# Kernel tuning notes

Measured on AMD Instinct MI355X. Metric: run time of the kernel, lower is better.

The kernel has to match this reference:

```python
import jax, jax.numpy as jnp
import numpy as np

D_HEAD = 64

def setup_inputs() -> dict:
    key = jax.random.key(0)
    ks = jax.random.split(key, 5)
    B, N, d_feat, d = 8, 2048, 256, 3
    f = jax.random.normal(ks[0], (B, N, d_feat), dtype=jnp.float32)
    x_tilde = jax.random.normal(ks[1], (B, N, d), dtype=jnp.float32)
    log_eps = jax.random.normal(ks[2], (B,), dtype=jnp.float32)
    W_q = jax.random.normal(ks[3], (d_feat + 1, D_HEAD), dtype=jnp.float32) * (1.0 / np.sqrt(d_feat + 1))
    W_k = jax.random.normal(ks[4], (d_feat + 1, D_HEAD), dtype=jnp.float32) * (1.0 / np.sqrt(d_feat + 1))
    return {"f": f, "x_tilde": x_tilde, "log_eps": log_eps, "W_q": W_q, "W_k": W_k}

def reference(f, x_tilde, log_eps, W_q, W_k):
    B, N, _ = f.shape
    # concat per-cloud log_eps scalar to every particle's features
    le = jnp.broadcast_to(log_eps[:, None, None], (B, N, 1)).astype(f.dtype)
    fc = jnp.concatenate([f, le], axis=-1)            # (B, N, d_feat+1)
    q = jnp.einsum('bnf,fh->bnh', fc, W_q)            # (B, N, d_head)
    k = jnp.einsum('bnf,fh->bnh', fc, W_k)            # (B, N, d_head)
    scale = jnp.asarray(np.sqrt(float(D_HEAD)), dtype=f.dtype)
    logits = jnp.einsum('bnh,bmh->bnm', q, k) / scale  # (B, N, N)
    N_f = jnp.asarray(N, dtype=f.dtype)
    col_softmax = jax.nn.softmax(logits, axis=1)       # softmax over QUERY axis
    pi = col_softmax / N_f                             # (B, N, N)
    # y_tilde = N * pi^T @ x_tilde
    y_tilde = N_f * jnp.einsum('bnm,bnd->bmd', pi, x_tilde)  # (B, N, d)
    return y_tilde, pi
```

## Files before the change

### kernel.cpp

```cpp
#include <hip/hip_runtime.h>
#include <hip/hip_bf16.h>

#define BB 8
#define NN 2048
#define DF 256
#define HH 64

using bf16x8 = __attribute__((ext_vector_type(8))) short;
using f32x4  = __attribute__((ext_vector_type(4))) float;
typedef unsigned short u16;

__global__ __launch_bounds__(256) void qk_proj_kernel(
    const float* __restrict__ f, const float* __restrict__ log_eps,
    const float* __restrict__ Wq, const float* __restrict__ Wk,
    __hip_bfloat16* __restrict__ Qs, __hip_bfloat16* __restrict__ Ks)
{
    __shared__ float wql[64 * 64];
    __shared__ float wkl[64 * 64];
    const int tid = threadIdx.x;
    const int h  = tid & 63;
    const int rg = tid >> 6;
    const int row_base = blockIdx.x * 32;
    const int b = row_base >> 11;

    const float le = log_eps[b];
    const float wq_last = Wq[DF * HH + h];
    const float wk_last = Wk[DF * HH + h];
    float q[8], k[8];
#pragma unroll
    for (int j = 0; j < 8; ++j) { q[j] = le * wq_last; k[j] = le * wk_last; }

    for (int kc = 0; kc < 4; ++kc) {
        __syncthreads();
#pragma unroll
        for (int it = 0; it < 4; ++it) {
            int idx = (tid + it * 256) * 4;
            *(float4*)&wql[idx] = *(const float4*)(Wq + kc * 4096 + idx);
            *(float4*)&wkl[idx] = *(const float4*)(Wk + kc * 4096 + idx);
        }
        __syncthreads();

        const float* fb = f + (size_t)(row_base + rg * 8) * DF + kc * 64;
#pragma unroll 4
        for (int i4 = 0; i4 < 16; ++i4) {
            float4 fv[8];
#pragma unroll
            for (int j = 0; j < 8; ++j)
                fv[j] = *(const float4*)(fb + (size_t)j * DF + i4 * 4);
#pragma unroll
            for (int u = 0; u < 4; ++u) {
                float wq = wql[(i4 * 4 + u) * 64 + h];
                float wk = wkl[(i4 * 4 + u) * 64 + h];
#pragma unroll
                for (int j = 0; j < 8; ++j) {
                    float fvv = (&fv[j].x)[u];
                    q[j] = fmaf(fvv, wq, q[j]);
                    k[j] = fmaf(fvv, wk, k[j]);
                }
            }
        }
    }

#pragma unroll
    for (int j = 0; j < 8; ++j) {
        int bn = row_base + rg * 8 + j;
        float qv = q[j] * 0.125f;
        float kv = k[j];
        __hip_bfloat16 qh = __float2bfloat16(qv);
        __hip_bfloat16 ql = __float2bfloat16(qv - __bfloat162float(qh));
        __hip_bfloat16 kh = __float2bfloat16(kv);
        __hip_bfloat16 kl = __float2bfloat16(kv - __bfloat162float(kh));
        size_t base = (size_t)bn * 128;
        Qs[base + h]      = qh;
        Qs[base + 64 + h] = ql;
        Ks[base + h]      = kh;
        Ks[base + 64 + h] = kl;
    }
}

__global__ __launch_bounds__(256) void attn_kernel(
    const u16* __restrict__ Qs, const u16* __restrict__ Ks,
    const float* __restrict__ x, float* __restrict__ y, float* __restrict__ pi)
{
    __shared__ float xs[NN * 3];
    __shared__ float cs_lds[32];
    __shared__ float yred[4 * 2 * 16 * 3];

    const int tid   = threadIdx.x;
    const int strip = blockIdx.x;
    const int b     = blockIdx.y;
    const int m0    = strip * 32;
    const int wave  = tid >> 6;
    const int lane  = tid & 63;
    const int l15   = lane & 15;
    const int quad  = lane >> 4;

    if (tid < 32) cs_lds[tid] = 0.f;
    for (int i = tid; i < NN * 3; i += 256) xs[i] = x[(size_t)b * NN * 3 + i];
    __syncthreads();

    bf16x8 bh[2][2], bl[2][2];
    {
        const u16* Kb = Ks + ((size_t)b * NN + m0) * 128;
#pragma unroll
        for (int ct = 0; ct < 2; ++ct) {
            const u16* kr = Kb + (size_t)(ct * 16 + l15) * 128;
#pragma unroll
            for (int ks = 0; ks < 2; ++ks) {
                int k0 = ks * 32 + quad * 8;
                bh[ct][ks] = *(const bf16x8*)(kr + k0);
                bl[ct][ks] = *(const bf16x8*)(kr + 64 + k0);
            }
        }
    }

    const u16* Qb = Qs + (size_t)b * NN * 128;
    float csacc0 = 0.f, csacc1 = 0.f;

    for (int rt = 0; rt < 16; ++rt) {
#pragma unroll
        for (int sr = 0; sr < 2; ++sr) {
            const int row0 = rt * 128 + wave * 32 + sr * 16;
            const u16* qr = Qb + (size_t)(row0 + l15) * 128;
            bf16x8 ah[2], al[2];
#pragma unroll
            for (int ks = 0; ks < 2; ++ks) {
                int k0 = ks * 32 + quad * 8;
                ah[ks] = *(const bf16x8*)(qr + k0);
                al[ks] = *(const bf16x8*)(qr + 64 + k0);
            }
#pragma unroll
            for (int ct = 0; ct < 2; ++ct) {
                f32x4 acc = {0.f, 0.f, 0.f, 0.f};
#pragma unroll
                for (int ks = 0; ks < 2; ++ks) {
                    acc = __builtin_amdgcn_mfma_f32_16x16x32_bf16(ah[ks], bh[ct][ks], acc, 0, 0, 0);
                    acc = __builtin_amdgcn_mfma_f32_16x16x32_bf16(ah[ks], bl[ct][ks], acc, 0, 0, 0);
                    acc = __builtin_amdgcn_mfma_f32_16x16x32_bf16(al[ks], bh[ct][ks], acc, 0, 0, 0);
                }
                float s = __expf(acc[0]) + __expf(acc[1]) + __expf(acc[2]) + __expf(acc[3]);
                s += __shfl_xor(s, 16);
                s += __shfl_xor(s, 32);
                if (ct == 0) csacc0 += s; else csacc1 += s;
            }
        }
    }
    if (quad == 0) {
        atomicAdd(&cs_lds[l15],      csacc0);
        atomicAdd(&cs_lds[16 + l15], csacc1);
    }
    __syncthreads();

    const float invc0 = 1.0f / cs_lds[l15];
    const float invc1 = 1.0f / cs_lds[16 + l15];
    const float invN  = 1.0f / (float)NN;
    float* pib = pi + (size_t)b * NN * NN + m0;
    float yacc[2][3] = {{0.f, 0.f, 0.f}, {0.f, 0.f, 0.f}};

    for (int rt = 0; rt < 16; ++rt) {
#pragma unroll
        for (int sr = 0; sr < 2; ++sr) {
            const int row0 = rt * 128 + wave * 32 + sr * 16;
            const u16* qr = Qb + (size_t)(row0 + l15) * 128;
            bf16x8 ah[2], al[2];
#pragma unroll
            for (int ks = 0; ks < 2; ++ks) {
                int k0 = ks * 32 + quad * 8;
                ah[ks] = *(const bf16x8*)(qr + k0);
                al[ks] = *(const bf16x8*)(qr + 64 + k0);
            }
            float xv[4][3];
#pragma unroll
            for (int r = 0; r < 4; ++r) {
                int row = row0 + quad * 4 + r;
                xv[r][0] = xs[row * 3 + 0];
                xv[r][1] = xs[row * 3 + 1];
                xv[r][2] = xs[row * 3 + 2];
            }
#pragma unroll
            for (int ct = 0; ct < 2; ++ct) {
                f32x4 acc = {0.f, 0.f, 0.f, 0.f};
#pragma unroll
                for (int ks = 0; ks < 2; ++ks) {
                    acc = __builtin_amdgcn_mfma_f32_16x16x32_bf16(ah[ks], bh[ct][ks], acc, 0, 0, 0);
                    acc = __builtin_amdgcn_mfma_f32_16x16x32_bf16(ah[ks], bl[ct][ks], acc, 0, 0, 0);
                    acc = __builtin_amdgcn_mfma_f32_16x16x32_bf16(al[ks], bh[ct][ks], acc, 0, 0, 0);
                }
                const float iv = (ct == 0) ? invc0 : invc1;
                float* op = pib + (size_t)(row0 + quad * 4) * NN + ct * 16 + l15;
#pragma unroll
                for (int r = 0; r < 4; ++r) {
                    float v = __expf(acc[r]) * iv;
                    op[(size_t)r * NN] = v * invN;
                    yacc[ct][0] = fmaf(v, xv[r][0], yacc[ct][0]);
                    yacc[ct][1] = fmaf(v, xv[r][1], yacc[ct][1]);
                    yacc[ct][2] = fmaf(v, xv[r][2], yacc[ct][2]);
                }
            }
        }
    }

#pragma unroll
    for (int ct = 0; ct < 2; ++ct)
#pragma unroll
        for (int d = 0; d < 3; ++d) {
            yacc[ct][d] += __shfl_xor(yacc[ct][d], 16);
            yacc[ct][d] += __shfl_xor(yacc[ct][d], 32);
        }
    if (quad == 0) {
#pragma unroll
        for (int ct = 0; ct < 2; ++ct)
#pragma unroll
            for (int d = 0; d < 3; ++d)
                yred[((wave * 2 + ct) * 16 + l15) * 3 + d] = yacc[ct][d];
    }
    __syncthreads();
    if (tid < 96) {
        int c = tid / 3, d = tid - c * 3;
        int ct = c >> 4, cl = c & 15;
        float s = 0.f;
#pragma unroll
        for (int w = 0; w < 4; ++w)
            s += yred[((w * 2 + ct) * 16 + cl) * 3 + d];
        y[((size_t)b * NN + m0 + c) * 3 + d] = s;
    }
}

extern "C" void kernel_launch(void* const* d_in, const int* in_sizes, int n_in,
                              void* d_out, int out_size, void* d_ws, size_t ws_size,
                              hipStream_t stream) {
    const float* f  = (const float*)d_in[0];
    const float* x  = (const float*)d_in[1];
    const float* le = (const float*)d_in[2];
    const float* Wq = (const float*)d_in[3];
    const float* Wk = (const float*)d_in[4];

    float* y  = (float*)d_out;
    float* pi = (float*)d_out + (size_t)BB * NN * 3;

    __hip_bfloat16* Qs = (__hip_bfloat16*)d_ws;
    __hip_bfloat16* Ks = Qs + (size_t)BB * NN * 128;

    qk_proj_kernel<<<dim3(BB * NN / 32), 256, 0, stream>>>(f, le, Wq, Wk, Qs, Ks);
    attn_kernel<<<dim3(64, BB), 256, 0, stream>>>((const u16*)Qs, (const u16*)Ks, x, y, pi);
}
```

Baseline: 240.2 us.

## Split attention into colsum and pi/y kernels over row tiles with atomics

The single attention kernel, which ran 512 blocks each looping over all query rows twice, becomes two kernels launched over 64x8xB grids. A colsum kernel accumulates column exp-sums into global memory with atomics, and a pi_y kernel recomputes logits per 256-row tile, writes pi as vectorized float4 stores along m, and atomically adds partial y. The MFMA operands are swapped so each lane owns contiguous columns for the wider stores. The projection kernel also halves its rows per block to launch more blocks. This adds two memsets, an extra launch and global atomics in exchange for much more parallelism and coalesced pi writes.

```diff
diff --git a/kernel.cpp b/kernel.cpp
--- a/kernel.cpp
+++ b/kernel.cpp
@@ -20,15 +20,15 @@
     const int tid = threadIdx.x;
     const int h  = tid & 63;
     const int rg = tid >> 6;
-    const int row_base = blockIdx.x * 32;
+    const int row_base = blockIdx.x * 16;
     const int b = row_base >> 11;
 
     const float le = log_eps[b];
     const float wq_last = Wq[DF * HH + h];
     const float wk_last = Wk[DF * HH + h];
-    float q[8], k[8];
-#pragma unroll
-    for (int j = 0; j < 8; ++j) { q[j] = le * wq_last; k[j] = le * wk_last; }
+    float q[4], k[4];
+#pragma unroll
+    for (int j = 0; j < 4; ++j) { q[j] = le * wq_last; k[j] = le * wk_last; }
 
     for (int kc = 0; kc < 4; ++kc) {
         __syncthreads();
@@ -40,19 +40,19 @@
         }
         __syncthreads();
 
-        const float* fb = f + (size_t)(row_base + rg * 8) * DF + kc * 64;
-#pragma unroll 4
+        const float* fb = f + (size_t)(row_base + rg * 4) * DF + kc * 64;
+#pragma unroll 8
         for (int i4 = 0; i4 < 16; ++i4) {
-            float4 fv[8];
-#pragma unroll
-            for (int j = 0; j < 8; ++j)
+            float4 fv[4];
+#pragma unroll
+            for (int j = 0; j < 4; ++j)
                 fv[j] = *(const float4*)(fb + (size_t)j * DF + i4 * 4);
 #pragma unroll
             for (int u = 0; u < 4; ++u) {
                 float wq = wql[(i4 * 4 + u) * 64 + h];
                 float wk = wkl[(i4 * 4 + u) * 64 + h];
 #pragma unroll
-                for (int j = 0; j < 8; ++j) {
+                for (int j = 0; j < 4; ++j) {
                     float fvv = (&fv[j].x)[u];
                     q[j] = fmaf(fvv, wq, q[j]);
                     k[j] = fmaf(fvv, wk, k[j]);
@@ -62,8 +62,8 @@
     }
 
 #pragma unroll
-    for (int j = 0; j < 8; ++j) {
-        int bn = row_base + rg * 8 + j;
+    for (int j = 0; j < 4; ++j) {
+        int bn = row_base + rg * 4 + j;
         float qv = q[j] * 0.125f;
         float kv = k[j];
         __hip_bfloat16 qh = __float2bfloat16(qv);
@@ -78,25 +78,21 @@
     }
 }
 
-__global__ __launch_bounds__(256) void attn_kernel(
+__global__ __launch_bounds__(256) void colsum_kernel(
     const u16* __restrict__ Qs, const u16* __restrict__ Ks,
-    const float* __restrict__ x, float* __restrict__ y, float* __restrict__ pi)
+    float* __restrict__ cs)
 {
-    __shared__ float xs[NN * 3];
     __shared__ float cs_lds[32];
-    __shared__ float yred[4 * 2 * 16 * 3];
-
-    const int tid   = threadIdx.x;
-    const int strip = blockIdx.x;
-    const int b     = blockIdx.y;
-    const int m0    = strip * 32;
-    const int wave  = tid >> 6;
-    const int lane  = tid & 63;
-    const int l15   = lane & 15;
-    const int quad  = lane >> 4;
+    const int tid  = threadIdx.x;
+    const int m0   = blockIdx.x * 32;
+    const int rt   = blockIdx.y;
+    const int b    = blockIdx.z;
+    const int wave = tid >> 6;
+    const int lane = tid & 63;
+    const int l15  = lane & 15;
+    const int quad = lane >> 4;
 
     if (tid < 32) cs_lds[tid] = 0.f;
-    for (int i = tid; i < NN * 3; i += 256) xs[i] = x[(size_t)b * NN * 3 + i];
     __syncthreads();
 
     bf16x8 bh[2][2], bl[2][2];
@@ -115,114 +111,156 @@
     }
 
     const u16* Qb = Qs + (size_t)b * NN * 128;
-    float csacc0 = 0.f, csacc1 = 0.f;
-
-    for (int rt = 0; rt < 16; ++rt) {
-#pragma unroll
-        for (int sr = 0; sr < 2; ++sr) {
-            const int row0 = rt * 128 + wave * 32 + sr * 16;
-            const u16* qr = Qb + (size_t)(row0 + l15) * 128;
-            bf16x8 ah[2], al[2];
+    float cs0 = 0.f, cs1 = 0.f;
+#pragma unroll
+    for (int sr = 0; sr < 4; ++sr) {
+        const int row0 = rt * 256 + wave * 64 + sr * 16;
+        const u16* qr = Qb + (size_t)(row0 + l15) * 128;
+        bf16x8 ah[2], al[2];
+#pragma unroll
+        for (int ks = 0; ks < 2; ++ks) {
+            int k0 = ks * 32 + quad * 8;
+            ah[ks] = *(const bf16x8*)(qr + k0);
+            al[ks] = *(const bf16x8*)(qr + 64 + k0);
+        }
+#pragma unroll
+        for (int ct = 0; ct < 2; ++ct) {
+            f32x4 acc = {0.f, 0.f, 0.f, 0.f};
+#pragma unroll
+            for (int ks = 0; ks < 2; ++ks) {
+                acc = __builtin_amdgcn_mfma_f32_16x16x32_bf16(ah[ks], bh[ct][ks], acc, 0, 0, 0);
+                acc = __builtin_amdgcn_mfma_f32_16x16x32_bf16(ah[ks], bl[ct][ks], acc, 0, 0, 0);
+                acc = __builtin_amdgcn_mfma_f32_16x16x32_bf16(al[ks], bh[ct][ks], acc, 0, 0, 0);
+            }
+            float s = __expf(acc[0]) + __expf(acc[1]) + __expf(acc[2]) + __expf(acc[3]);
+            s += __shfl_xor(s, 16);
+            s += __shfl_xor(s, 32);
+            if (ct == 0) cs0 += s; else cs1 += s;
+        }
+    }
+    if (quad == 0) {
+        atomicAdd(&cs_lds[l15],      cs0);
+        atomicAdd(&cs_lds[16 + l15], cs1);
+    }
+    __syncthreads();
+    if (tid < 32) atomicAdd(&cs[(size_t)b * NN + m0 + tid], cs_lds[tid]);
+}
+
+__global__ __launch_bounds__(256) void pi_y_kernel(
+    const u16* __restrict__ Qs, const u16* __restrict__ Ks,
+    const float* __restrict__ x, const float* __restrict__ cs,
+    float* __restrict__ y, float* __restrict__ pi)
+{
+    __shared__ float xt[256 * 3];
+    __shared__ float iv_lds[32], ivn_lds[32];
+    __shared__ float yred[4][32][3];
+
+    const int tid  = threadIdx.x;
+    const int m0   = blockIdx.x * 32;
+    const int rt   = blockIdx.y;
+    const int b    = blockIdx.z;
+    const int n0   = rt * 256;
+    const int wave = tid >> 6;
+    const int lane = tid & 63;
+    const int l15  = lane & 15;
+    const int quad = lane >> 4;
+
+    for (int i = tid; i < 256 * 3; i += 256) xt[i] = x[((size_t)b * NN + n0) * 3 + i];
+    if (tid < 32) {
+        float iv = 1.0f / cs[(size_t)b * NN + m0 + tid];
+        iv_lds[tid]  = iv;
+        ivn_lds[tid] = iv * (1.0f / (float)NN);
+    }
+    __syncthreads();
+
+    bf16x8 kh[2][2], kl[2][2];
+    {
+        const u16* Kb = Ks + ((size_t)b * NN + m0) * 128;
+#pragma unroll
+        for (int ct = 0; ct < 2; ++ct) {
+            const u16* kr = Kb + (size_t)(ct * 16 + l15) * 128;
 #pragma unroll
             for (int ks = 0; ks < 2; ++ks) {
                 int k0 = ks * 32 + quad * 8;
-                ah[ks] = *(const bf16x8*)(qr + k0);
-                al[ks] = *(const bf16x8*)(qr + 64 + k0);
-            }
-#pragma unroll
-            for (int ct = 0; ct < 2; ++ct) {
-                f32x4 acc = {0.f, 0.f, 0.f, 0.f};
-#pragma unroll
-                for (int ks = 0; ks < 2; ++ks) {
-                    acc = __builtin_amdgcn_mfma_f32_16x16x32_bf16(ah[ks], bh[ct][ks], acc, 0, 0, 0);
-                    acc = __builtin_amdgcn_mfma_f32_16x16x32_bf16(ah[ks], bl[ct][ks], acc, 0, 0, 0);
-                    acc = __builtin_amdgcn_mfma_f32_16x16x32_bf16(al[ks], bh[ct][ks], acc, 0, 0, 0);
-                }
-                float s = __expf(acc[0]) + __expf(acc[1]) + __expf(acc[2]) + __expf(acc[3]);
-                s += __shfl_xor(s, 16);
-                s += __shfl_xor(s, 32);
-                if (ct == 0) csacc0 += s; else csacc1 += s;
-            }
-        }
-    }
-    if (quad == 0) {
-        atomicAdd(&cs_lds[l15],      csacc0);
-        atomicAdd(&cs_lds[16 + l15], csacc1);
-    }
-    __syncthreads();
-
-    const float invc0 = 1.0f / cs_lds[l15];
-    const float invc1 = 1.0f / cs_lds[16 + l15];
-    const float invN  = 1.0f / (float)NN;
-    float* pib = pi + (size_t)b * NN * NN + m0;
-    float yacc[2][3] = {{0.f, 0.f, 0.f}, {0.f, 0.f, 0.f}};
-
-    for (int rt = 0; rt < 16; ++rt) {
-#pragma unroll
-        for (int sr = 0; sr < 2; ++sr) {
-            const int row0 = rt * 128 + wave * 32 + sr * 16;
-            const u16* qr = Qb + (size_t)(row0 + l15) * 128;
-            bf16x8 ah[2], al[2];
-#pragma unroll
-            for (int ks = 0; ks < 2; ++ks) {
-                int k0 = ks * 32 + quad * 8;
-                ah[ks] = *(const bf16x8*)(qr + k0);
-                al[ks] = *(const bf16x8*)(qr + 64 + k0);
-            }
-            float xv[4][3];
+                kh[ct][ks] = *(const bf16x8*)(kr + k0);
+                kl[ct][ks] = *(const bf16x8*)(kr + 64 + k0);
+            }
+        }
+    }
+
+    const u16* Qb = Qs + (size_t)b * NN * 128;
+    float yacc[2][4][3];
+#pragma unroll
+    for (int ct = 0; ct < 2; ++ct)
+#pragma unroll
+        for (int r = 0; r < 4; ++r)
+#pragma unroll
+            for (int d = 0; d < 3; ++d) yacc[ct][r][d] = 0.f;
+
+#pragma unroll
+    for (int sr = 0; sr < 4; ++sr) {
+        const int nloc = wave * 64 + sr * 16 + l15;
+        const u16* qr = Qb + (size_t)(n0 + nloc) * 128;
+        bf16x8 qh[2], ql[2];
+#pragma unroll
+        for (int ks = 0; ks < 2; ++ks) {
+            int k0 = ks * 32 + quad * 8;
+            qh[ks] = *(const bf16x8*)(qr + k0);
+            ql[ks] = *(const bf16x8*)(qr + 64 + k0);
+        }
+        const float xv0 = xt[nloc * 3 + 0];
+        const float xv1 = xt[nloc * 3 + 1];
+        const float xv2 = xt[nloc * 3 + 2];
+#pragma unroll
+        for (int ct = 0; ct < 2; ++ct) {
+            f32x4 acc = {0.f, 0.f, 0.f, 0.f};
+#pragma unroll
+            for (int ks = 0; ks < 2; ++ks) {
+                acc = __builtin_amdgcn_mfma_f32_16x16x32_bf16(kh[ct][ks], qh[ks], acc, 0, 0, 0);
+                acc = __builtin_amdgcn_mfma_f32_16x16x32_bf16(kh[ct][ks], ql[ks], acc, 0, 0, 0);
+                acc = __builtin_amdgcn_mfma_f32_16x16x32_bf16(kl[ct][ks], qh[ks], acc, 0, 0, 0);
+            }
+            const int mloc = ct * 16 + quad * 4;
+            f32x4 pv;
 #pragma unroll
             for (int r = 0; r < 4; ++r) {
-                int row = row0 + quad * 4 + r;
-                xv[r][0] = xs[row * 3 + 0];
-                xv[r][1] = xs[row * 3 + 1];
-                xv[r][2] = xs[row * 3 + 2];
-            }
-#pragma unroll
-            for (int ct = 0; ct < 2; ++ct) {
-                f32x4 acc = {0.f, 0.f, 0.f, 0.f};
-#pragma unroll
-                for (int ks = 0; ks < 2; ++ks) {
-                    acc = __builtin_amdgcn_mfma_f32_16x16x32_bf16(ah[ks], bh[ct][ks], acc, 0, 0, 0);
-                    acc = __builtin_amdgcn_mfma_f32_16x16x32_bf16(ah[ks], bl[ct][ks], acc, 0, 0, 0);
-                    acc = __builtin_amdgcn_mfma_f32_16x16x32_bf16(al[ks], bh[ct][ks], acc, 0, 0, 0);
-                }
-                const float iv = (ct == 0) ? invc0 : invc1;
-                float* op = pib + (size_t)(row0 + quad * 4) * NN + ct * 16 + l15;
-#pragma unroll
-                for (int r = 0; r < 4; ++r) {
-                    float v = __expf(acc[r]) * iv;
-                    op[(size_t)r * NN] = v * invN;
-                    yacc[ct][0] = fmaf(v, xv[r][0], yacc[ct][0]);
-                    yacc[ct][1] = fmaf(v, xv[r][1], yacc[ct][1]);
-                    yacc[ct][2] = fmaf(v, xv[r][2], yacc[ct][2]);
-                }
-            }
+                float e = __expf(acc[r]);
+                pv[r] = e * ivn_lds[mloc + r];
+                yacc[ct][r][0] = fmaf(e, xv0, yacc[ct][r][0]);
+                yacc[ct][r][1] = fmaf(e, xv1, yacc[ct][r][1]);
+                yacc[ct][r][2] = fmaf(e, xv2, yacc[ct][r][2]);
+            }
+            *(f32x4*)(pi + ((size_t)b * NN + n0 + nloc) * NN + m0 + mloc) = pv;
         }
     }
 
 #pragma unroll
     for (int ct = 0; ct < 2; ++ct)
 #pragma unroll
-        for (int d = 0; d < 3; ++d) {
-            yacc[ct][d] += __shfl_xor(yacc[ct][d], 16);
-            yacc[ct][d] += __shfl_xor(yacc[ct][d], 32);
-        }
-    if (quad == 0) {
+        for (int r = 0; r < 4; ++r)
+#pragma unroll
+            for (int d = 0; d < 3; ++d) {
+                float v = yacc[ct][r][d];
+                v += __shfl_xor(v, 1);
+                v += __shfl_xor(v, 2);
+                v += __shfl_xor(v, 4);
+                v += __shfl_xor(v, 8);
+                yacc[ct][r][d] = v;
+            }
+    if (l15 == 0) {
 #pragma unroll
         for (int ct = 0; ct < 2; ++ct)
 #pragma unroll
-            for (int d = 0; d < 3; ++d)
-                yred[((wave * 2 + ct) * 16 + l15) * 3 + d] = yacc[ct][d];
+            for (int r = 0; r < 4; ++r)
+#pragma unroll
+                for (int d = 0; d < 3; ++d)
+                    yred[wave][ct * 16 + quad * 4 + r][d] = yacc[ct][r][d];
     }
     __syncthreads();
     if (tid < 96) {
         int c = tid / 3, d = tid - c * 3;
-        int ct = c >> 4, cl = c & 15;
-        float s = 0.f;
-#pragma unroll
-        for (int w = 0; w < 4; ++w)
-            s += yred[((w * 2 + ct) * 16 + cl) * 3 + d];
-        y[((size_t)b * NN + m0 + c) * 3 + d] = s;
+        float s = yred[0][c][d] + yred[1][c][d] + yred[2][c][d] + yred[3][c][d];
+        atomicAdd(&y[((size_t)b * NN + m0 + c) * 3 + d], s * iv_lds[c]);
     }
 }
 
@@ -240,7 +278,12 @@
 
     __hip_bfloat16* Qs = (__hip_bfloat16*)d_ws;
     __hip_bfloat16* Ks = Qs + (size_t)BB * NN * 128;
-
-    qk_proj_kernel<<<dim3(BB * NN / 32), 256, 0, stream>>>(f, le, Wq, Wk, Qs, Ks);
-    attn_kernel<<<dim3(64, BB), 256, 0, stream>>>((const u16*)Qs, (const u16*)Ks, x, y, pi);
-}
+    float* cs = (float*)((char*)d_ws + 16u * 1024 * 1024);
+
+    hipMemsetAsync(cs, 0, (size_t)BB * NN * sizeof(float), stream);
+    hipMemsetAsync(y,  0, (size_t)BB * NN * 3 * sizeof(float), stream);
+
+    qk_proj_kernel<<<dim3(BB * NN / 16), 256, 0, stream>>>(f, le, Wq, Wk, Qs, Ks);
+    colsum_kernel<<<dim3(64, 8, BB), 256, 0, stream>>>((const u16*)Qs, (const u16*)Ks, cs);
+    pi_y_kernel<<<dim3(64, 8, BB), 256, 0, stream>>>((const u16*)Qs, (const u16*)Ks, x, cs, y, pi);
+}
```

Result: slower. 286.1 us (+19.1%).
